# Performance work log

Hardware: AMD Instinct MI355X
Metric: run time of the kernel (lower is better)

The kernel has to match this reference:

```python
import jax, jax.numpy as jnp
import numpy as np

B, S, D, H = 4, 2048, 1024, 16
HD = D // H  # head_size = 64


def setup_inputs() -> dict:
    key = jax.random.key(0)
    ks = jax.random.split(key, 9)
    sc = 0.02
    x = jax.random.normal(ks[0], (B, S, D), dtype=jnp.float32)
    Wq = jax.random.normal(ks[1], (H, D, HD), dtype=jnp.float32) * sc
    Wk = jax.random.normal(ks[2], (H, D, HD), dtype=jnp.float32) * sc
    Wv = jax.random.normal(ks[3], (H, D, HD), dtype=jnp.float32) * sc
    bq = jax.random.normal(ks[4], (H, HD), dtype=jnp.float32) * sc
    bk = jax.random.normal(ks[5], (H, HD), dtype=jnp.float32) * sc
    bv = jax.random.normal(ks[6], (H, HD), dtype=jnp.float32) * sc
    Wp = jax.random.normal(ks[7], (D, D), dtype=jnp.float32) * sc
    bp = jax.random.normal(ks[8], (D,), dtype=jnp.float32) * sc
    return {"x": x, "Wq": Wq, "bq": bq, "Wk": Wk, "bk": bk,
            "Wv": Wv, "bv": bv, "Wp": Wp, "bp": bp}


def reference(x, Wq, bq, Wk, bk, Wv, bv, Wp, bp):
    # Per-head Linear q/k/v, batched over heads with einsum (equivalent math
    # to the original Python loop over SingleHeadAttention modules).
    q = jnp.einsum('bsd,hde->bhse', x, Wq) + bq[None, :, None, :]
    k = jnp.einsum('bsd,hde->bhse', x, Wk) + bk[None, :, None, :]
    v = jnp.einsum('bsd,hde->bhse', x, Wv) + bv[None, :, None, :]
    att = jnp.einsum('bhqe,bhke->bhqk', q, k) / jnp.sqrt(jnp.asarray(HD, q.dtype))
    causal = jnp.tril(jnp.ones((S, S), dtype=bool))  # [S,S]
    att = jnp.where(causal[None, None], att, jnp.finfo(att.dtype).min)
    w = jax.nn.softmax(att, axis=-1)
    o = jnp.einsum('bhqk,bhke->bhqe', w, v)           # [B,H,S,HD]
    o = o.transpose(0, 2, 1, 3).reshape(B, S, D)      # concat heads on last dim
    # output projection; dropout is identity in eval (p=0.0)
    return jnp.einsum('bsd,de->bse', o, Wp) + bp
```

## Files before the change

### kernel.cpp

```cpp
#include <hip/hip_runtime.h>
#include <hip/hip_bf16.h>

typedef __attribute__((ext_vector_type(8)))  short bf16x8;
typedef __attribute__((ext_vector_type(4)))  float f32x4;
typedef __attribute__((ext_vector_type(16))) float f32x16;
typedef __attribute__((ext_vector_type(2)))  int   i32x2;

#define NH  16
#define HD  64
#define SEQ 2048
#define DM  1024
#define NB  4

#define QSCALE 0.18033688011112042f

#define MFMA(a,b,c)   __builtin_amdgcn_mfma_f32_16x16x32_bf16((a),(b),(c),0,0,0)
#define MFMA32(a,b,c) __builtin_amdgcn_mfma_f32_32x32x16_bf16((a),(b),(c),0,0,0)

static __device__ __forceinline__ void gload_lds16(const void* g, void* l) {
    __builtin_amdgcn_global_load_lds(
        (const __attribute__((address_space(1))) void*)g,
        (__attribute__((address_space(3))) void*)l, 16, 0, 0);
}

__global__ __launch_bounds__(256)
void prep(const float* __restrict__ x,  const float* __restrict__ Wq,
          const float* __restrict__ Wk, const float* __restrict__ Wv,
          const float* __restrict__ Wp,
          __hip_bfloat16* __restrict__ xb,  __hip_bfloat16* __restrict__ wqt,
          __hip_bfloat16* __restrict__ wkt, __hip_bfloat16* __restrict__ wvt,
          __hip_bfloat16* __restrict__ wpt) {
    const long XE = (long)NB * SEQ * DM;
    const long CAST_T = XE / 8;
    long gid = (long)blockIdx.x * 256 + threadIdx.x;
    if (gid < CAST_T) {
        long i = gid * 8;
        float4 a = *reinterpret_cast<const float4*>(x + i);
        float4 b = *reinterpret_cast<const float4*>(x + i + 4);
        ushort4 o1, o2;
        o1.x = __bfloat16_as_ushort(__float2bfloat16(a.x));
        o1.y = __bfloat16_as_ushort(__float2bfloat16(a.y));
        o1.z = __bfloat16_as_ushort(__float2bfloat16(a.z));
        o1.w = __bfloat16_as_ushort(__float2bfloat16(a.w));
        o2.x = __bfloat16_as_ushort(__float2bfloat16(b.x));
        o2.y = __bfloat16_as_ushort(__float2bfloat16(b.y));
        o2.z = __bfloat16_as_ushort(__float2bfloat16(b.z));
        o2.w = __bfloat16_as_ushort(__float2bfloat16(b.w));
        *reinterpret_cast<ushort4*>(xb + i)     = o1;
        *reinterpret_cast<ushort4*>(xb + i + 4) = o2;
        return;
    }
    long r = gid - CAST_T;
    const long WQK = 1 << 20;
    if (r < 3 * WQK) {
        int z = (int)(r >> 20);
        long idx = r & (WQK - 1);
        const float* src = (z == 0) ? Wq : (z == 1) ? Wk : Wv;
        __hip_bfloat16* dst = (z == 0) ? wqt : (z == 1) ? wkt : wvt;
        int c  = (int)(idx & 63);
        long t2 = idx >> 6;
        int rr = (int)(t2 & 1023);
        int mm = (int)(t2 >> 10);
        dst[((long)mm * HD + c) * DM + rr] = __float2bfloat16(src[idx]);
    } else {
        long idx = r - 3 * WQK;
        int c  = (int)(idx & 1023);
        int rr = (int)(idx >> 10);
        wpt[(long)c * DM + rr] = __float2bfloat16(Wp[idx]);
    }
}

__global__ __launch_bounds__(256)
void qkv_gemm(const __hip_bfloat16* __restrict__ A,
              const __hip_bfloat16* __restrict__ BT,
              const float* __restrict__ b0,
              const float* __restrict__ b1,
              const float* __restrict__ b2,
              __hip_bfloat16* __restrict__ Qo,
              __hip_bfloat16* __restrict__ Ko,
              __hip_bfloat16* __restrict__ Vto) {
    __shared__ __align__(16) char lds[2][32768];
    int tid = threadIdx.x;
    int w = tid >> 6, l = tid & 63;
    int lr = l & 15, lg = l >> 4;
    int wr = w >> 1, wc = w & 1;
    int mtile = blockIdx.x, ntile = blockIdx.y;
    const int AR0 = mtile * 128, BR0 = ntile * 128;

    const int rsub = w * 8 + (l >> 3);
    const int sg0 = l & 7;
    auto stage = [&](const __hip_bfloat16* g, int grow0, int kc, char* lbase) {
#pragma unroll
        for (int i = 0; i < 4; ++i) {
            int row = i * 32 + rsub;
            gload_lds16(g + (long)(grow0 + row) * DM + kc + ((sg0 ^ (row & 7)) << 3),
                        lbase + i * 4096 + w * 1024);
        }
    };

    int aoff[4][2], boff[4][2];
#pragma unroll
    for (int m = 0; m < 4; ++m) {
        int ra = wr * 64 + m * 16 + lr;
        int rb = wc * 64 + m * 16 + lr;
#pragma unroll
        for (int kh = 0; kh < 2; ++kh) {
            aoff[m][kh] = ra * 128 + (((kh * 4 + lg) ^ (ra & 7)) << 4);
            boff[m][kh] = 16384 + rb * 128 + (((kh * 4 + lg) ^ (rb & 7)) << 4);
        }
    }

    f32x4 acc[4][4] = {};

    stage(A,  AR0, 0, lds[0]);
    stage(BT, BR0, 0, lds[0] + 16384);
    __syncthreads();

    int cur = 0;
    for (int kt = 0; kt < 16; ++kt) {
        if (kt < 15) {
            int kc = (kt + 1) * 64;
            stage(A,  AR0, kc, lds[cur ^ 1]);
            stage(BT, BR0, kc, lds[cur ^ 1] + 16384);
        }
        bf16x8 bf[4][2];
#pragma unroll
        for (int n = 0; n < 4; ++n) {
            bf[n][0] = *(const bf16x8*)(lds[cur] + boff[n][0]);
            bf[n][1] = *(const bf16x8*)(lds[cur] + boff[n][1]);
        }
#pragma unroll
        for (int m = 0; m < 4; ++m) {
            bf16x8 a0 = *(const bf16x8*)(lds[cur] + aoff[m][0]);
            bf16x8 a1 = *(const bf16x8*)(lds[cur] + aoff[m][1]);
#pragma unroll
            for (int n = 0; n < 4; ++n) {
                acc[m][n] = MFMA(a0, bf[n][0], acc[m][n]);
                acc[m][n] = MFMA(a1, bf[n][1], acc[m][n]);
            }
        }
        __syncthreads();
        cur ^= 1;
    }

    int z = ntile >> 3;
    const float* bias = (z == 0) ? b0 : (z == 1) ? b1 : b2;
    int colbase = (ntile & 7) * 128 + wc * 64;
#pragma unroll
    for (int n = 0; n < 4; ++n) {
        int hc = colbase + n * 16 + lr;
        int h = hc >> 6, e = hc & 63;
        float bb = bias[hc];
#pragma unroll
        for (int m = 0; m < 4; ++m) {
            int row0 = mtile * 128 + wr * 64 + m * 16 + lg * 4;
            int b = row0 >> 11, s0 = row0 & 2047;
            if (z == 0) {
#pragma unroll
                for (int r = 0; r < 4; ++r)
                    Qo[(((long)b * NH + h) * SEQ + s0 + r) * HD + e] =
                        __float2bfloat16((acc[m][n][r] + bb) * QSCALE);
            } else if (z == 1) {
#pragma unroll
                for (int r = 0; r < 4; ++r)
                    Ko[(((long)b * NH + h) * SEQ + s0 + r) * HD + e] =
                        __float2bfloat16(acc[m][n][r] + bb);
            } else {
                ushort4 s4;
                s4.x = __bfloat16_as_ushort(__float2bfloat16(acc[m][n][0] + bb));
                s4.y = __bfloat16_as_ushort(__float2bfloat16(acc[m][n][1] + bb));
                s4.z = __bfloat16_as_ushort(__float2bfloat16(acc[m][n][2] + bb));
                s4.w = __bfloat16_as_ushort(__float2bfloat16(acc[m][n][3] + bb));
                *reinterpret_cast<ushort4*>(
                    Vto + ((long)(b * NH + h) * HD + e) * SEQ + s0) = s4;
            }
        }
    }
}

__global__ __launch_bounds__(256)
void out_gemm(const __hip_bfloat16* __restrict__ A,
              const __hip_bfloat16* __restrict__ BT,
              const float* __restrict__ b0,
              float* __restrict__ Fo) {
    __shared__ __align__(16) char lds[2][32768];
    int tid = threadIdx.x;
    int w = tid >> 6, l = tid & 63;
    int lr = l & 15, lg = l >> 4;
    int wr = w >> 1, wc = w & 1;
    int mtile = blockIdx.x, ntile = blockIdx.y;
    const int AR0 = mtile * 128, BR0 = ntile * 128;

    const int rsub = w * 8 + (l >> 3);
    const int sg0 = l & 7;
    auto stage = [&](const __hip_bfloat16* g, int grow0, int kc, char* lbase) {
#pragma unroll
        for (int i = 0; i < 4; ++i) {
            int row = i * 32 + rsub;
            gload_lds16(g + (long)(grow0 + row) * DM + kc + ((sg0 ^ (row & 7)) << 3),
                        lbase + i * 4096 + w * 1024);
        }
    };

    int aoff[4][2], boff[4][2];
#pragma unroll
    for (int m = 0; m < 4; ++m) {
        int ra = wr * 64 + m * 16 + lr;
        int rb = wc * 64 + m * 16 + lr;
#pragma unroll
        for (int kh = 0; kh < 2; ++kh) {
            aoff[m][kh] = ra * 128 + (((kh * 4 + lg) ^ (ra & 7)) << 4);
            boff[m][kh] = 16384 + rb * 128 + (((kh * 4 + lg) ^ (rb & 7)) << 4);
        }
    }

    f32x4 acc[4][4] = {};

    stage(A,  AR0, 0, lds[0]);
    stage(BT, BR0, 0, lds[0] + 16384);
    __syncthreads();

    int cur = 0;
    for (int kt = 0; kt < 16; ++kt) {
        if (kt < 15) {
            int kc = (kt + 1) * 64;
            stage(A,  AR0, kc, lds[cur ^ 1]);
            stage(BT, BR0, kc, lds[cur ^ 1] + 16384);
        }
        bf16x8 bf[4][2];
#pragma unroll
        for (int n = 0; n < 4; ++n) {
            bf[n][0] = *(const bf16x8*)(lds[cur] + boff[n][0]);
            bf[n][1] = *(const bf16x8*)(lds[cur] + boff[n][1]);
        }
#pragma unroll
        for (int m = 0; m < 4; ++m) {
            bf16x8 a0 = *(const bf16x8*)(lds[cur] + aoff[m][0]);
            bf16x8 a1 = *(const bf16x8*)(lds[cur] + aoff[m][1]);
#pragma unroll
            for (int n = 0; n < 4; ++n) {
                acc[m][n] = MFMA(a0, bf[n][0], acc[m][n]);
                acc[m][n] = MFMA(a1, bf[n][1], acc[m][n]);
            }
        }
        __syncthreads();
        cur ^= 1;
    }

#pragma unroll
    for (int n = 0; n < 4; ++n) {
        int col = ntile * 128 + wc * 64 + n * 16 + lr;
        float bb = b0[col];
#pragma unroll
        for (int m = 0; m < 4; ++m) {
            long row0 = mtile * 128 + wr * 64 + m * 16 + lg * 4;
#pragma unroll
            for (int r = 0; r < 4; ++r)
                Fo[(row0 + r) * DM + col] = acc[m][n][r] + bb;
        }
    }
}

static __device__ __forceinline__ unsigned pkbf(float a, float b) {
    __hip_bfloat162 h = __float22bfloat162_rn(float2{a, b});
    union { __hip_bfloat162 h2; unsigned u; } u_; u_.h2 = h;
    return u_.u;
}
static __device__ __forceinline__ bf16x8 make_pb(unsigned w0, unsigned w1,
                                                 unsigned w2, unsigned w3) {
    union { unsigned u[4]; bf16x8 v; } u_;
    u_.u[0] = w0; u_.u[1] = w1; u_.u[2] = w2; u_.u[3] = w3;
    return u_.v;
}
static __device__ __forceinline__ i32x2 pl32swap(unsigned a, unsigned b) {
    return __builtin_amdgcn_permlane32_swap((int)a, (int)b, false, false);
}
static __device__ __forceinline__ float xsum32(float x) {
    i32x2 r = pl32swap(__float_as_uint(x), __float_as_uint(x));
    return __uint_as_float((unsigned)r[0]) + __uint_as_float((unsigned)r[1]);
}

template<bool MASKED>
static __device__ __forceinline__ void attn_tile(
    const bf16x8* kf, const bf16x8* qf, const bf16x8* vf,
    int lo5, int hi,
    f32x16& o0, f32x16& o1, float& lsum) {
    f32x16 st = {};
    __builtin_amdgcn_s_setprio(1);
#pragma unroll
    for (int kd = 0; kd < 4; ++kd) st = MFMA32(kf[kd], qf[kd], st);
    __builtin_amdgcn_s_setprio(0);
    if (MASKED) {
#pragma unroll
        for (int r = 0; r < 16; ++r) {
            int kvloc = (r & 3) + 8 * (r >> 2) + 4 * hi;
            st[r] = (kvloc > lo5) ? -INFINITY : st[r];
        }
    }
    float p[16];
#pragma unroll
    for (int r = 0; r < 16; ++r) p[r] = __builtin_amdgcn_exp2f(st[r]);
    float s0 = (p[0] + p[1]) + (p[2] + p[3]);
    float s1 = (p[4] + p[5]) + (p[6] + p[7]);
    float s2 = (p[8] + p[9]) + (p[10] + p[11]);
    float s3 = (p[12] + p[13]) + (p[14] + p[15]);
    lsum += (s0 + s1) + (s2 + s3);

    unsigned pk0 = pkbf(p[0],  p[1]),  pk1 = pkbf(p[2],  p[3]);
    unsigned pk2 = pkbf(p[4],  p[5]),  pk3 = pkbf(p[6],  p[7]);
    unsigned pk4 = pkbf(p[8],  p[9]),  pk5 = pkbf(p[10], p[11]);
    unsigned pk6 = pkbf(p[12], p[13]), pk7 = pkbf(p[14], p[15]);
    i32x2 s02 = pl32swap(pk0, pk2);
    i32x2 s13 = pl32swap(pk1, pk3);
    i32x2 s46 = pl32swap(pk4, pk6);
    i32x2 s57 = pl32swap(pk5, pk7);
    bf16x8 pb0 = make_pb((unsigned)s02[0], (unsigned)s13[0],
                         (unsigned)s02[1], (unsigned)s13[1]);
    bf16x8 pb1 = make_pb((unsigned)s46[0], (unsigned)s57[0],
                         (unsigned)s46[1], (unsigned)s57[1]);

    __builtin_amdgcn_s_setprio(1);
    o0 = MFMA32(vf[0], pb0, o0);
    o1 = MFMA32(vf[1], pb0, o1);
    o0 = MFMA32(vf[2], pb1, o0);
    o1 = MFMA32(vf[3], pb1, o1);
    __builtin_amdgcn_s_setprio(0);
}

__global__ __launch_bounds__(256)
void flash_attn(const __hip_bfloat16* __restrict__ Q,
                const __hip_bfloat16* __restrict__ K,
                const __hip_bfloat16* __restrict__ Vt,
                __hip_bfloat16* __restrict__ O) {
    __shared__ __align__(16) char kv[2][8192];
    int bh = blockIdx.x;
    int w  = threadIdx.x >> 6, l = threadIdx.x & 63;
    int lo5 = l & 31, hi = l >> 5;
    int y  = blockIdx.y;
    int pr = y * 4 + w;
    int jA = pr, jB = 63 - pr;
    int q0A = jA * 32, q0B = jB * 32;
    const int TMAX = 63 - 4 * y;

    const __hip_bfloat16* Qh = Q  + (long)bh * SEQ * HD;
    const __hip_bfloat16* Kh = K  + (long)bh * SEQ * HD;
    const __hip_bfloat16* Vh = Vt + (long)bh * HD * SEQ;

    bf16x8 qfA[4], qfB[4];
#pragma unroll
    for (int kd = 0; kd < 4; ++kd) {
        qfA[kd] = *reinterpret_cast<const bf16x8*>(
            Qh + (long)(q0A + lo5) * HD + kd * 16 + hi * 8);
        qfB[kd] = *reinterpret_cast<const bf16x8*>(
            Qh + (long)(q0B + lo5) * HD + kd * 16 + hi * 8);
    }

    int srow = w * 8 + (l >> 3);
    int kslot = (l & 7) ^ (srow & 7);
    const __hip_bfloat16* ksrc = Kh + (long)srow * HD + kslot * 8;
    int vlog = (l & 7) ^ (srow & 7);
    int vrow = srow + ((vlog >> 2) << 5);
    const __hip_bfloat16* vsrc = Vh + (long)vrow * SEQ + (vlog & 3) * 8;

    int ka[4], va[4];
#pragma unroll
    for (int kd = 0; kd < 4; ++kd)
        ka[kd] = lo5 * 128 + (((kd * 2 + hi) ^ (lo5 & 7)) << 4);
    va[0] = 4096 + lo5 * 128 + (((0 + hi) ^ (lo5 & 7)) << 4);
    va[1] = 4096 + lo5 * 128 + (((4 + hi) ^ (lo5 & 7)) << 4);
    va[2] = 4096 + lo5 * 128 + (((2 + hi) ^ (lo5 & 7)) << 4);
    va[3] = 4096 + lo5 * 128 + (((6 + hi) ^ (lo5 & 7)) << 4);

    f32x16 oA0 = {}, oA1 = {}, oB0 = {}, oB1 = {};
    float lsA = 0.f, lsB = 0.f;

    gload_lds16(ksrc, kv[0] + w * 1024);
    gload_lds16(vsrc, kv[0] + 4096 + w * 1024);
    __syncthreads();

    int buf = 0;
    for (int t = 0; t <= TMAX; ++t) {
        if (t < TMAX) {
            gload_lds16(ksrc + (long)(t + 1) * 32 * HD, kv[buf ^ 1] + w * 1024);
            gload_lds16(vsrc + (t + 1) * 32,            kv[buf ^ 1] + 4096 + w * 1024);
        }
        const char* cb = kv[buf];
        bf16x8 kf[4], vf[4];
#pragma unroll
        for (int kd = 0; kd < 4; ++kd)
            kf[kd] = *reinterpret_cast<const bf16x8*>(cb + ka[kd]);
#pragma unroll
        for (int j = 0; j < 4; ++j)
            vf[j] = *reinterpret_cast<const bf16x8*>(cb + va[j]);

        if (t < jA) {
            attn_tile<false>(kf, qfB, vf, lo5, hi, oB0, oB1, lsB);
            attn_tile<false>(kf, qfA, vf, lo5, hi, oA0, oA1, lsA);
        } else if (t == jA) {
            attn_tile<true >(kf, qfA, vf, lo5, hi, oA0, oA1, lsA);
            attn_tile<false>(kf, qfB, vf, lo5, hi, oB0, oB1, lsB);
        } else if (t < jB) {
            attn_tile<false>(kf, qfB, vf, lo5, hi, oB0, oB1, lsB);
        } else if (t == jB) {
            attn_tile<true >(kf, qfB, vf, lo5, hi, oB0, oB1, lsB);
        }
        __syncthreads();
        buf ^= 1;
    }

    int b = bh >> 4, h = bh & 15;
    float invA = 1.0f / xsum32(lsA);
    float invB = 1.0f / xsum32(lsB);
#pragma unroll
    for (int c = 0; c < 2; ++c) {
        int q0 = c ? q0B : q0A;
        const f32x16& o0 = c ? oB0 : oA0;
        const f32x16& o1 = c ? oB1 : oA1;
        float inv = c ? invB : invA;
        __hip_bfloat16* orow = O + ((long)b * SEQ + q0 + lo5) * DM + h * HD;
#pragma unroll
        for (int nd = 0; nd < 2; ++nd) {
#pragma unroll
            for (int rg = 0; rg < 4; ++rg) {
                ushort4 s4;
                float a0 = (nd ? o1[rg * 4 + 0] : o0[rg * 4 + 0]) * inv;
                float a1 = (nd ? o1[rg * 4 + 1] : o0[rg * 4 + 1]) * inv;
                float a2 = (nd ? o1[rg * 4 + 2] : o0[rg * 4 + 2]) * inv;
                float a3 = (nd ? o1[rg * 4 + 3] : o0[rg * 4 + 3]) * inv;
                s4.x = __bfloat16_as_ushort(__float2bfloat16(a0));
                s4.y = __bfloat16_as_ushort(__float2bfloat16(a1));
                s4.z = __bfloat16_as_ushort(__float2bfloat16(a2));
                s4.w = __bfloat16_as_ushort(__float2bfloat16(a3));
                *reinterpret_cast<ushort4*>(orow + nd * 32 + rg * 8 + hi * 4) = s4;
            }
        }
    }
}

extern "C" void kernel_launch(void* const* d_in, const int* in_sizes, int n_in,
                              void* d_out, int out_size, void* d_ws, size_t ws_size,
                              hipStream_t stream) {
    const float* x  = (const float*)d_in[0];
    const float* Wq = (const float*)d_in[1];
    const float* bq = (const float*)d_in[2];
    const float* Wk = (const float*)d_in[3];
    const float* bk = (const float*)d_in[4];
    const float* Wv = (const float*)d_in[5];
    const float* bv = (const float*)d_in[6];
    const float* Wp = (const float*)d_in[7];
    const float* bp = (const float*)d_in[8];
    float* out = (float*)d_out;

    char* ws = (char*)d_ws;
    const long XE = (long)NB * SEQ * DM;
    const long QKV_ELEMS = (long)NB * NH * SEQ * HD;
    __hip_bfloat16* xb   = (__hip_bfloat16*)ws; ws += XE * 2;
    __hip_bfloat16* Qws  = (__hip_bfloat16*)ws; ws += QKV_ELEMS * 2;
    __hip_bfloat16* Kws  = (__hip_bfloat16*)ws; ws += QKV_ELEMS * 2;
    __hip_bfloat16* Vtws = (__hip_bfloat16*)ws; ws += QKV_ELEMS * 2;
    __hip_bfloat16* Ows  = (__hip_bfloat16*)ws; ws += QKV_ELEMS * 2;
    __hip_bfloat16* wqt  = (__hip_bfloat16*)ws; ws += (long)NH * DM * HD * 2;
    __hip_bfloat16* wkt  = (__hip_bfloat16*)ws; ws += (long)NH * DM * HD * 2;
    __hip_bfloat16* wvt  = (__hip_bfloat16*)ws; ws += (long)NH * DM * HD * 2;
    __hip_bfloat16* wpt  = (__hip_bfloat16*)ws; ws += (long)DM * DM * 2;

    prep<<<20480, 256, 0, stream>>>(x, Wq, Wk, Wv, Wp, xb, wqt, wkt, wvt, wpt);

    qkv_gemm<<<dim3(64, 24), 256, 0, stream>>>(
        xb, wqt, bq, bk, bv, Qws, Kws, Vtws);

    flash_attn<<<dim3(64, 8), 256, 0, stream>>>(Qws, Kws, Vtws, Ows);

    out_gemm<<<dim3(64, 8), 256, 0, stream>>>(Ows, wpt, bp, out);
}
```

Before: 179.3 us.

## Split KV tiles across wave pairs in flash attention and merge partials via LDS

Each pair of waves now shares one pair of query row-blocks, and the two waves take alternating KV tiles (split-K). Their partial outputs and row sums are combined through shared memory at the end. The grid doubles to 64x16 so more blocks are in flight. The softmax appears to use a fixed max with no running-max rescale, so the partials add directly. The cost is extra LDS (about 33KB) and a reduction step, and each wave does half the work per loaded tile, which may lower occupancy.

```diff
diff --git a/kernel.cpp b/kernel.cpp
--- a/kernel.cpp
+++ b/kernel.cpp
@@ -333,14 +333,17 @@
                 const __hip_bfloat16* __restrict__ Vt,
                 __hip_bfloat16* __restrict__ O) {
     __shared__ __align__(16) char kv[2][8192];
+    __shared__ float mbuf[2][66][64];
     int bh = blockIdx.x;
     int w  = threadIdx.x >> 6, l = threadIdx.x & 63;
     int lo5 = l & 31, hi = l >> 5;
     int y  = blockIdx.y;
-    int pr = y * 4 + w;
+    int p  = w >> 1;
+    int h  = w & 1;
+    int pr = y * 2 + p;
     int jA = pr, jB = 63 - pr;
     int q0A = jA * 32, q0B = jB * 32;
-    const int TMAX = 63 - 4 * y;
+    const int TMAX = 63 - 2 * y;
 
     const __hip_bfloat16* Qh = Q  + (long)bh * SEQ * HD;
     const __hip_bfloat16* Kh = K  + (long)bh * SEQ * HD;
@@ -384,31 +387,57 @@
             gload_lds16(ksrc + (long)(t + 1) * 32 * HD, kv[buf ^ 1] + w * 1024);
             gload_lds16(vsrc + (t + 1) * 32,            kv[buf ^ 1] + 4096 + w * 1024);
         }
-        const char* cb = kv[buf];
-        bf16x8 kf[4], vf[4];
-#pragma unroll
-        for (int kd = 0; kd < 4; ++kd)
-            kf[kd] = *reinterpret_cast<const bf16x8*>(cb + ka[kd]);
-#pragma unroll
-        for (int j = 0; j < 4; ++j)
-            vf[j] = *reinterpret_cast<const bf16x8*>(cb + va[j]);
-
-        if (t < jA) {
-            attn_tile<false>(kf, qfB, vf, lo5, hi, oB0, oB1, lsB);
-            attn_tile<false>(kf, qfA, vf, lo5, hi, oA0, oA1, lsA);
-        } else if (t == jA) {
-            attn_tile<true >(kf, qfA, vf, lo5, hi, oA0, oA1, lsA);
-            attn_tile<false>(kf, qfB, vf, lo5, hi, oB0, oB1, lsB);
-        } else if (t < jB) {
-            attn_tile<false>(kf, qfB, vf, lo5, hi, oB0, oB1, lsB);
-        } else if (t == jB) {
-            attn_tile<true >(kf, qfB, vf, lo5, hi, oB0, oB1, lsB);
+        if (((t & 1) == h) && t <= jB) {
+            const char* cb = kv[buf];
+            bf16x8 kf[4], vf[4];
+#pragma unroll
+            for (int kd = 0; kd < 4; ++kd)
+                kf[kd] = *reinterpret_cast<const bf16x8*>(cb + ka[kd]);
+#pragma unroll
+            for (int j = 0; j < 4; ++j)
+                vf[j] = *reinterpret_cast<const bf16x8*>(cb + va[j]);
+
+            if (t < jA) {
+                attn_tile<false>(kf, qfB, vf, lo5, hi, oB0, oB1, lsB);
+                attn_tile<false>(kf, qfA, vf, lo5, hi, oA0, oA1, lsA);
+            } else if (t == jA) {
+                attn_tile<true >(kf, qfA, vf, lo5, hi, oA0, oA1, lsA);
+                attn_tile<false>(kf, qfB, vf, lo5, hi, oB0, oB1, lsB);
+            } else if (t < jB) {
+                attn_tile<false>(kf, qfB, vf, lo5, hi, oB0, oB1, lsB);
+            } else {
+                attn_tile<true >(kf, qfB, vf, lo5, hi, oB0, oB1, lsB);
+            }
         }
         __syncthreads();
         buf ^= 1;
     }
 
-    int b = bh >> 4, h = bh & 15;
+    if (h == 1) {
+#pragma unroll
+        for (int r = 0; r < 16; ++r) {
+            mbuf[p][r][l]      = oA0[r];
+            mbuf[p][16 + r][l] = oA1[r];
+            mbuf[p][32 + r][l] = oB0[r];
+            mbuf[p][48 + r][l] = oB1[r];
+        }
+        mbuf[p][64][l] = lsA;
+        mbuf[p][65][l] = lsB;
+    }
+    __syncthreads();
+    if (h == 1) return;
+
+#pragma unroll
+    for (int r = 0; r < 16; ++r) {
+        oA0[r] += mbuf[p][r][l];
+        oA1[r] += mbuf[p][16 + r][l];
+        oB0[r] += mbuf[p][32 + r][l];
+        oB1[r] += mbuf[p][48 + r][l];
+    }
+    lsA += mbuf[p][64][l];
+    lsB += mbuf[p][65][l];
+
+    int b = bh >> 4, hh = bh & 15;
     float invA = 1.0f / xsum32(lsA);
     float invB = 1.0f / xsum32(lsB);
 #pragma unroll
@@ -417,7 +446,7 @@
         const f32x16& o0 = c ? oB0 : oA0;
         const f32x16& o1 = c ? oB1 : oA1;
         float inv = c ? invB : invA;
-        __hip_bfloat16* orow = O + ((long)b * SEQ + q0 + lo5) * DM + h * HD;
+        __hip_bfloat16* orow = O + ((long)b * SEQ + q0 + lo5) * DM + hh * HD;
 #pragma unroll
         for (int nd = 0; nd < 2; ++nd) {
 #pragma unroll
@@ -469,7 +498,7 @@
     qkv_gemm<<<dim3(64, 24), 256, 0, stream>>>(
         xb, wqt, bq, bk, bv, Qws, Kws, Vtws);
 
-    flash_attn<<<dim3(64, 8), 256, 0, stream>>>(Qws, Kws, Vtws, Ows);
+    flash_attn<<<dim3(64, 16), 256, 0, stream>>>(Qws, Kws, Vtws, Ows);
 
     out_gemm<<<dim3(64, 8), 256, 0, stream>>>(Ows, wpt, bp, out);
 }
```

Result: slower. 216.6 us (+20.8%).
